# Optimization experiments

Hardware: AMD Instinct MI355X
Metric: run time of the kernel (lower is better)

The kernel has to match this reference:

```python
import jax, jax.numpy as jnp
import numpy as np

N_LAYERS = 24  # number of recurrent applications of the shared HashLinear


def setup_inputs() -> dict:
    key = jax.random.key(0)
    ks = jax.random.split(key, 9)
    B, D_IN, N, N_OUT = 1024, 784, 4096, 10
    s_in = 1.0 / np.sqrt(D_IN)
    s_h = 1.0 / np.sqrt(N)
    x = jax.random.normal(ks[0], (B, D_IN), jnp.float32)
    # nn.Linear(prod(input_dim), 2*n_units)
    W_in = jax.random.uniform(ks[1], (2 * N, D_IN), jnp.float32, -s_in, s_in)
    b_in = jax.random.uniform(ks[2], (2 * N,), jnp.float32, -s_in, s_in)
    # HashLinear(n_units, n_units, period=1, 'hash'): learnable +/-1 context key + shared linear
    key_sp = jnp.where(jax.random.bernoulli(ks[3], 0.5, (1, N)), 1.0, -1.0).astype(jnp.float32)
    W_sp = jax.random.uniform(ks[4], (N, N), jnp.float32, -s_h, s_h)
    b_sp = jax.random.uniform(ks[5], (N,), jnp.float32, -s_h, s_h)
    # HashLinear(n_units, 10, period=1, 'hash')
    key_f = jnp.where(jax.random.bernoulli(ks[6], 0.5, (1, N)), 1.0, -1.0).astype(jnp.float32)
    W_f = jax.random.uniform(ks[7], (N_OUT, N), jnp.float32, -s_h, s_h)
    b_f = jax.random.uniform(ks[8], (N_OUT,), jnp.float32, -s_h, s_h)
    return {"x": x, "W_in": W_in, "b_in": b_in, "key_sp": key_sp, "W_sp": W_sp,
            "b_sp": b_sp, "key_f": key_f, "W_f": W_f, "b_f": b_f, "time": 0}


def _hash_linear(xa, xb, o, W, b):
    # Superposition HashLinear: same shared weight applied to both streams,
    # each modulated by the +/-1 context key o ([n_in]).
    ya = (xa * o) @ W.T + b
    yb = (xb * o) @ W.T + b
    return ya, yb


def reference(x, W_in, b_in, key_sp, W_sp, b_sp, key_f, W_f, b_f, time):
    N = W_sp.shape[0]
    r = x @ W_in.T + b_in                 # [B, 2N]
    r_a, r_b = r[:, :N], r[:, N:]         # torch.split(r, n_units, 1)
    pre0 = r_a
    r_a, r_b = jax.nn.relu(r_a), jax.nn.relu(r_b)
    o = key_sp[time % key_sp.shape[0]]    # period=1, time=0 in the module

    def step(carry, _):
        a, b2 = carry
        ya, yb = _hash_linear(a, b2, o, W_sp, b_sp)
        return (jax.nn.relu(ya), jax.nn.relu(yb)), ya  # collect preactivation r_a

    (r_a, r_b), pres = jax.lax.scan(step, (r_a, r_b), None, length=N_LAYERS)
    of = key_f[time % key_f.shape[0]]
    out_a, out_b = _hash_linear(r_a, r_b, of, W_f, b_f)  # [B,10], [B,10]
    preactivations = jnp.concatenate([pre0[None], pres], axis=0)  # [N_LAYERS+1, B, N]
    return (out_a, out_b, preactivations)
```

## Files before the change

kernel.cpp:

```cpp
#include <hip/hip_runtime.h>
#include <hip/hip_bf16.h>
#include <stdint.h>

typedef __bf16 bf16x8 __attribute__((ext_vector_type(8)));
typedef float  f32x4  __attribute__((ext_vector_type(4)));

#define NH      4096
#define MB      1024
#define M2      2048
#define DIN     784
#define KPAD    832
#define N_IN    8192
#define NLAYERS 24
#define NOUT    10

#define ASLOT   (256 * 64)
#define BSLOT   (128 * 64)
#define SLOT    (ASLOT + BSLOT)

__device__ __forceinline__ unsigned short f2bf(float x) {
  union { float f; unsigned u; } v; v.f = x;
  unsigned r = v.u + 0x7FFFu + ((v.u >> 16) & 1u);
  return (unsigned short)(r >> 16);
}
__device__ __forceinline__ float bf2f(unsigned short u) {
  union { unsigned u; float f; } v; v.u = ((unsigned)u) << 16; return v.f;
}

__device__ __forceinline__ void async16(const void* g, void* l) {
  __builtin_amdgcn_global_load_lds(
      (const __attribute__((address_space(1))) void*)g,
      (__attribute__((address_space(3))) void*)l, 16, 0, 0);
}

__global__ void k_conv_wsp(const float* __restrict__ W, const float* __restrict__ o,
                           unsigned short* __restrict__ out) {
  size_t i = ((size_t)blockIdx.x * blockDim.x + threadIdx.x) * 4;
  if (i >= (size_t)NH * NH) return;
  float4 w = *reinterpret_cast<const float4*>(W + i);
  int k = (int)(i & (NH - 1));
  float4 ov = *reinterpret_cast<const float4*>(o + k);
  ushort4 r;
  r.x = f2bf(w.x * ov.x); r.y = f2bf(w.y * ov.y);
  r.z = f2bf(w.z * ov.z); r.w = f2bf(w.w * ov.w);
  *reinterpret_cast<ushort4*>(out + i) = r;
}

__global__ void k_conv_pad(const float* __restrict__ in, unsigned short* __restrict__ out,
                           int rows, int kin, int kout) {
  size_t i = (size_t)blockIdx.x * blockDim.x + threadIdx.x;
  if (i >= (size_t)rows * kout) return;
  int r = (int)(i / kout), c = (int)(i % kout);
  out[i] = (c < kin) ? f2bf(in[(size_t)r * kin + c]) : (unsigned short)0;
}

__device__ __forceinline__ void gemm_core(
    const unsigned short* __restrict__ Ag, const unsigned short* __restrict__ Bg,
    int K, int bm, int bn, unsigned short* lds, f32x4 acc[4][4])
{
  const int t    = threadIdx.x;
  const int lane = t & 63;
  const int wave = t >> 6;
  const int wm   = wave >> 1;
  const int wn   = wave & 1;
  const int l15  = lane & 15;
  const int lkb  = (lane >> 4) * 16;

  const int srow = t >> 3;
  const int sb   = ((t & 7) * 16) ^ ((srow & 7) << 4);
  const unsigned aG0 = (unsigned)((bm + srow) * K + (sb >> 1));
  const unsigned bG0 = (unsigned)((bn + srow) * K + (sb >> 1));

  auto STAGE = [&](int slotIdx, int k0) {
    unsigned short* s = lds + slotIdx * SLOT;
#pragma unroll
    for (int j = 0; j < 4; ++j)
      async16(Ag + aG0 + (unsigned)(j * 64 * K + k0), s + t * 8 + j * 4096);
#pragma unroll
    for (int j = 0; j < 2; ++j)
      async16(Bg + bG0 + (unsigned)(j * 64 * K + k0), s + ASLOT + t * 8 + j * 4096);
  };

  int aRd[2][4], bRd[2][4];
#pragma unroll
  for (int kk = 0; kk < 2; ++kk)
#pragma unroll
    for (int i = 0; i < 4; ++i) {
      const int ra = wm * 64 + i * 16 + l15;
      aRd[kk][i] = (ra * 128 + ((kk * 64 + lkb) ^ ((ra & 7) << 4))) >> 1;
      const int rb = wn * 64 + i * 16 + l15;
      bRd[kk][i] = (rb * 128 + ((kk * 64 + lkb) ^ ((rb & 7) << 4))) >> 1;
    }

  bf16x8 aX[4], bX[4], aY[4], bY[4];

  auto READS = [&](int slotIdx, int kk, bf16x8* A4, bf16x8* B4) {
    const unsigned short* base = lds + slotIdx * SLOT;
#pragma unroll
    for (int i = 0; i < 4; ++i) A4[i] = *reinterpret_cast<const bf16x8*>(base + aRd[kk][i]);
#pragma unroll
    for (int i = 0; i < 4; ++i) B4[i] = *reinterpret_cast<const bf16x8*>(base + ASLOT + bRd[kk][i]);
  };
  auto MM = [&](const bf16x8* A4, const bf16x8* B4) {
    __builtin_amdgcn_s_setprio(1);
#pragma unroll
    for (int mi = 0; mi < 4; ++mi)
#pragma unroll
      for (int ni = 0; ni < 4; ++ni)
        acc[mi][ni] = __builtin_amdgcn_mfma_f32_16x16x32_bf16(A4[mi], B4[ni], acc[mi][ni], 0, 0, 0);
    __builtin_amdgcn_s_setprio(0);
  };

  const int nt = K >> 6;
  STAGE(0, 0);
  STAGE(1, 64);
  asm volatile("s_waitcnt vmcnt(6)" ::: "memory");
  __builtin_amdgcn_s_barrier();
  __builtin_amdgcn_sched_barrier(0);
  READS(0, 0, aX, bX);

  int s0 = 0, s1 = 1, s2 = 2;
  for (int kt = 0; kt < nt; ++kt) {
    if (kt + 2 < nt) STAGE(s2, (kt + 2) << 6);
    READS(s0, 1, aY, bY);
    MM(aX, bX);
    __builtin_amdgcn_sched_barrier(0);
    asm volatile("s_waitcnt lgkmcnt(0)" ::: "memory");
    __builtin_amdgcn_sched_barrier(0);
    if (kt + 1 < nt) {
      if (kt + 2 < nt) asm volatile("s_waitcnt vmcnt(6)" ::: "memory");
      else             asm volatile("s_waitcnt vmcnt(0)" ::: "memory");
      __builtin_amdgcn_s_barrier();
      __builtin_amdgcn_sched_barrier(0);
      READS(s1, 0, aX, bX);
    }
    MM(aY, bY);
    const int n0 = s1, n1 = s2, n2 = s0;
    s0 = n0; s1 = n1; s2 = n2;
  }
}

__global__ __launch_bounds__(512, 2) void k_gemm_layer(
    const unsigned short* __restrict__ A, const unsigned short* __restrict__ W,
    const float* __restrict__ bias, float* __restrict__ preact,
    unsigned short* __restrict__ Anext)
{
  __shared__ __align__(16) unsigned short lds[3 * SLOT];
  const int bid = blockIdx.x;
  const int s   = ((bid & 7) << 5) + (bid >> 3);
  const int bm = (s >> 5) * 256;
  const int bn = (s & 31) * 128;
  f32x4 acc[4][4] = {};
  gemm_core(A, W, NH, bm, bn, lds, acc);

  const int lane = threadIdx.x & 63;
  const int wave = threadIdx.x >> 6;
  const int wm = (wave >> 1) * 64, wn = (wave & 1) * 64;
  const int l15 = lane & 15;
#pragma unroll
  for (int mi = 0; mi < 4; ++mi) {
    const int gm0 = bm + wm + mi * 16 + (lane >> 4) * 4;
#pragma unroll
    for (int ni = 0; ni < 4; ++ni) {
      const int gn = bn + wn + ni * 16 + l15;
      const float bv = bias[gn];
#pragma unroll
      for (int r = 0; r < 4; ++r) {
        const int gm = gm0 + r;
        const float y = acc[mi][ni][r] + bv;
        if (gm < MB) preact[(size_t)gm * NH + gn] = y;
        Anext[(size_t)gm * NH + gn] = f2bf(y > 0.f ? y : 0.f);
      }
    }
  }
}

__global__ __launch_bounds__(512, 2) void k_gemm_in(
    const unsigned short* __restrict__ X, const unsigned short* __restrict__ W,
    const float* __restrict__ bias, float* __restrict__ preact0,
    unsigned short* __restrict__ A0)
{
  __shared__ __align__(16) unsigned short lds[3 * SLOT];
  const int bid = blockIdx.x;
  const int s   = ((bid & 7) << 5) + (bid >> 3);
  const int bm = (s >> 6) * 256;
  const int bn = (s & 63) * 128;
  f32x4 acc[4][4] = {};
  gemm_core(X, W, KPAD, bm, bn, lds, acc);

  const int lane = threadIdx.x & 63;
  const int wave = threadIdx.x >> 6;
  const int wm = (wave >> 1) * 64, wn = (wave & 1) * 64;
  const int l15 = lane & 15;
#pragma unroll
  for (int mi = 0; mi < 4; ++mi) {
    const int gm0 = bm + wm + mi * 16 + (lane >> 4) * 4;
#pragma unroll
    for (int ni = 0; ni < 4; ++ni) {
      const int gn = bn + wn + ni * 16 + l15;
      const float bv = bias[gn];
#pragma unroll
      for (int r = 0; r < 4; ++r) {
        const int gm = gm0 + r;
        const float y = acc[mi][ni][r] + bv;
        const unsigned short rl = f2bf(y > 0.f ? y : 0.f);
        if (gn < NH) {
          preact0[(size_t)gm * NH + gn] = y;
          A0[(size_t)gm * NH + gn] = rl;
        } else {
          A0[(size_t)(MB + gm) * NH + (gn - NH)] = rl;
        }
      }
    }
  }
}

__global__ void k_final(const unsigned short* __restrict__ A,
                        const float* __restrict__ Wf, const float* __restrict__ of,
                        const float* __restrict__ bf_, float* __restrict__ out)
{
  const int m = blockIdx.x;
  const int t = threadIdx.x;
  float accj[NOUT] = {};
  for (int k = t; k < NH; k += 256) {
    const float a = bf2f(A[(size_t)m * NH + k]) * of[k];
#pragma unroll
    for (int j = 0; j < NOUT; ++j) accj[j] += a * Wf[j * NH + k];
  }
  __shared__ float red[4][NOUT];
#pragma unroll
  for (int j = 0; j < NOUT; ++j) {
    float v = accj[j];
    for (int off = 32; off > 0; off >>= 1) v += __shfl_down(v, off);
    if ((t & 63) == 0) red[t >> 6][j] = v;
  }
  __syncthreads();
  if (t < NOUT) {
    const float s = red[0][t] + red[1][t] + red[2][t] + red[3][t] + bf_[t];
    out[(size_t)m * NOUT + t] = s;
  }
}

extern "C" void kernel_launch(void* const* d_in, const int* in_sizes, int n_in,
                              void* d_out, int out_size, void* d_ws, size_t ws_size,
                              hipStream_t stream) {
  const float* x     = (const float*)d_in[0];
  const float* W_in  = (const float*)d_in[1];
  const float* b_in  = (const float*)d_in[2];
  const float* keysp = (const float*)d_in[3];
  const float* W_sp  = (const float*)d_in[4];
  const float* b_sp  = (const float*)d_in[5];
  const float* keyf  = (const float*)d_in[6];
  const float* W_f   = (const float*)d_in[7];
  const float* b_f   = (const float*)d_in[8];

  float* out    = (float*)d_out;
  float* preact = out + (size_t)2 * MB * NOUT;

  char* ws = (char*)d_ws;
  unsigned short* Wsp_bf = (unsigned short*)ws;  ws += (size_t)NH * NH * 2;
  unsigned short* A0     = (unsigned short*)ws;  ws += (size_t)M2 * NH * 2;
  unsigned short* A1     = (unsigned short*)ws;  ws += (size_t)M2 * NH * 2;
  unsigned short* Win_bf = (unsigned short*)ws;  ws += (size_t)N_IN * KPAD * 2;
  unsigned short* X_bf   = (unsigned short*)ws;  ws += (size_t)MB * KPAD * 2;

  k_conv_wsp<<<(NH * (size_t)NH / 4 + 255) / 256, 256, 0, stream>>>(W_sp, keysp, Wsp_bf);
  k_conv_pad<<<((size_t)N_IN * KPAD + 255) / 256, 256, 0, stream>>>(W_in, Win_bf, N_IN, DIN, KPAD);
  k_conv_pad<<<((size_t)MB * KPAD + 255) / 256, 256, 0, stream>>>(x, X_bf, MB, DIN, KPAD);

  k_gemm_in<<<256, 512, 0, stream>>>(X_bf, Win_bf, b_in, preact, A0);

  unsigned short* Ain = A0;
  unsigned short* Aout = A1;
  for (int tlay = 0; tlay < NLAYERS; ++tlay) {
    float* pre = preact + (size_t)(tlay + 1) * MB * NH;
    k_gemm_layer<<<256, 512, 0, stream>>>(Ain, Wsp_bf, b_sp, pre, Aout);
    unsigned short* tmp = Ain; Ain = Aout; Aout = tmp;
  }

  k_final<<<M2, 256, 0, stream>>>(Ain, W_f, keyf, b_f, out);
}
```

Before: 1.670 ms.

## Restructure GEMM main loop into barrier-synchronized half-tile phases with split staging

The k-loop of the shared bf16 MFMA GEMM core is rescheduled. The previous software pipeline preloaded the next half-tile's LDS reads into registers while MFMAs ran. The new loop splits each 64-wide k-tile into two phases, and each phase issues its LDS reads, half of the async global-to-LDS staging for a later tile, a barrier, and then the 16 MFMAs, followed by another barrier. This spreads the global loads across the MFMA phases and lowers register pressure, but it adds barriers and no longer overlaps LDS reads with the previous MFMA block.

Measured after the change: 1.739 ms. 1.04x slower.

```diff
diff --git a/kernel.cpp b/kernel.cpp
--- a/kernel.cpp
+++ b/kernel.cpp
@@ -71,14 +71,12 @@
   const unsigned aG0 = (unsigned)((bm + srow) * K + (sb >> 1));
   const unsigned bG0 = (unsigned)((bn + srow) * K + (sb >> 1));
 
-  auto STAGE = [&](int slotIdx, int k0) {
+  auto STAGE_P = [&](int slotIdx, int k0, int part) {
     unsigned short* s = lds + slotIdx * SLOT;
-#pragma unroll
-    for (int j = 0; j < 4; ++j)
-      async16(Ag + aG0 + (unsigned)(j * 64 * K + k0), s + t * 8 + j * 4096);
-#pragma unroll
-    for (int j = 0; j < 2; ++j)
-      async16(Bg + bG0 + (unsigned)(j * 64 * K + k0), s + ASLOT + t * 8 + j * 4096);
+    const int ja = part * 2;
+    async16(Ag + aG0 + (unsigned)((ja + 0) * 64 * K + k0), s + t * 8 + (ja + 0) * 4096);
+    async16(Ag + aG0 + (unsigned)((ja + 1) * 64 * K + k0), s + t * 8 + (ja + 1) * 4096);
+    async16(Bg + bG0 + (unsigned)(part * 64 * K + k0), s + ASLOT + t * 8 + part * 4096);
   };
 
   int aRd[2][4], bRd[2][4];
@@ -92,51 +90,42 @@
       bRd[kk][i] = (rb * 128 + ((kk * 64 + lkb) ^ ((rb & 7) << 4))) >> 1;
     }
 
-  bf16x8 aX[4], bX[4], aY[4], bY[4];
-
-  auto READS = [&](int slotIdx, int kk, bf16x8* A4, bf16x8* B4) {
-    const unsigned short* base = lds + slotIdx * SLOT;
-#pragma unroll
-    for (int i = 0; i < 4; ++i) A4[i] = *reinterpret_cast<const bf16x8*>(base + aRd[kk][i]);
-#pragma unroll
-    for (int i = 0; i < 4; ++i) B4[i] = *reinterpret_cast<const bf16x8*>(base + ASLOT + bRd[kk][i]);
-  };
-  auto MM = [&](const bf16x8* A4, const bf16x8* B4) {
-    __builtin_amdgcn_s_setprio(1);
-#pragma unroll
-    for (int mi = 0; mi < 4; ++mi)
-#pragma unroll
-      for (int ni = 0; ni < 4; ++ni)
-        acc[mi][ni] = __builtin_amdgcn_mfma_f32_16x16x32_bf16(A4[mi], B4[ni], acc[mi][ni], 0, 0, 0);
-    __builtin_amdgcn_s_setprio(0);
-  };
-
   const int nt = K >> 6;
-  STAGE(0, 0);
-  STAGE(1, 64);
+  STAGE_P(0, 0, 0);  STAGE_P(0, 0, 1);
+  STAGE_P(1, 64, 0); STAGE_P(1, 64, 1);
   asm volatile("s_waitcnt vmcnt(6)" ::: "memory");
   __builtin_amdgcn_s_barrier();
-  __builtin_amdgcn_sched_barrier(0);
-  READS(0, 0, aX, bX);
-
-  int s0 = 0, s1 = 1, s2 = 2;
+
+  int s0 = 0, s2 = 2;
   for (int kt = 0; kt < nt; ++kt) {
-    if (kt + 2 < nt) STAGE(s2, (kt + 2) << 6);
-    READS(s0, 1, aY, bY);
-    MM(aX, bX);
-    __builtin_amdgcn_sched_barrier(0);
-    asm volatile("s_waitcnt lgkmcnt(0)" ::: "memory");
-    __builtin_amdgcn_sched_barrier(0);
-    if (kt + 1 < nt) {
-      if (kt + 2 < nt) asm volatile("s_waitcnt vmcnt(6)" ::: "memory");
-      else             asm volatile("s_waitcnt vmcnt(0)" ::: "memory");
+    const unsigned short* base = lds + s0 * SLOT;
+#pragma unroll
+    for (int half = 0; half < 2; ++half) {
+      bf16x8 A4[4], B4[4];
+#pragma unroll
+      for (int i = 0; i < 4; ++i) A4[i] = *reinterpret_cast<const bf16x8*>(base + aRd[half][i]);
+#pragma unroll
+      for (int i = 0; i < 4; ++i) B4[i] = *reinterpret_cast<const bf16x8*>(base + ASLOT + bRd[half][i]);
+      if (kt + 2 < nt) STAGE_P(s2, (kt + 2) << 6, half);
+      if (half == 1) {
+        if (kt + 2 < nt)      asm volatile("s_waitcnt vmcnt(6)" ::: "memory");
+        else if (kt + 1 < nt) asm volatile("s_waitcnt vmcnt(0)" ::: "memory");
+      }
       __builtin_amdgcn_s_barrier();
+      asm volatile("s_waitcnt lgkmcnt(0)" ::: "memory");
       __builtin_amdgcn_sched_barrier(0);
-      READS(s1, 0, aX, bX);
-    }
-    MM(aY, bY);
-    const int n0 = s1, n1 = s2, n2 = s0;
-    s0 = n0; s1 = n1; s2 = n2;
+      __builtin_amdgcn_s_setprio(1);
+#pragma unroll
+      for (int mi = 0; mi < 4; ++mi)
+#pragma unroll
+        for (int ni = 0; ni < 4; ++ni)
+          acc[mi][ni] = __builtin_amdgcn_mfma_f32_16x16x32_bf16(A4[mi], B4[ni], acc[mi][ni], 0, 0, 0);
+      __builtin_amdgcn_s_setprio(0);
+      __builtin_amdgcn_s_barrier();
+    }
+    const int ns0 = (s0 == 2) ? 0 : s0 + 1;
+    const int ns2 = (s2 == 2) ? 0 : s2 + 1;
+    s0 = ns0; s2 = ns2;
   }
 }
 
```
